# Performance work log

Measured on AMD Instinct MI355X. Metric: run time of the kernel, lower is better.

The kernel has to match this reference:

```python
import jax, jax.numpy as jnp
import numpy as np
from jax import lax

H, I, N, R, K, B, L = 2048, 4096, 16, 128, 4, 1, 2048

def silu(v):
    return v * jax.nn.sigmoid(v)

def setup_inputs() -> dict:
    key = jax.random.key(0)
    ks = jax.random.split(key, 8)
    f = jnp.float32
    x = jax.random.normal(ks[0], (B, L, H), f)
    W_in = jax.random.normal(ks[1], (H, 2 * I), f) / np.sqrt(H).astype(np.float32)
    conv_w = jax.random.normal(ks[2], (I, 1, K), f) / np.sqrt(K).astype(np.float32)  # OIH depthwise
    conv_b = jnp.zeros((I,), f)
    W_x = jax.random.normal(ks[3], (I, R + 2 * N), f) / np.sqrt(I).astype(np.float32)
    W_dt = jax.random.normal(ks[4], (R, I), f) / np.sqrt(R).astype(np.float32)
    # dt bias init as in Mamba: inverse-softplus of log-uniform dt
    dt = jnp.clip(jnp.exp(jax.random.normal(ks[5], (I,), f) * (np.log(0.1) - np.log(0.001)).astype(np.float32) + np.float32(np.log(0.001))), 1e-4, 0.1)
    b_dt = dt + jnp.log(-jnp.expm1(-dt))
    W_out = jax.random.normal(ks[6], (I, H), f) / np.sqrt(I).astype(np.float32)
    A_log = jnp.log(jnp.broadcast_to(jnp.arange(1, N + 1, dtype=f), (I, N)))
    D = jnp.ones((I,), f)
    return {"x": x, "W_in": W_in, "conv_w": conv_w, "conv_b": conv_b, "W_x": W_x,
            "W_dt": W_dt, "b_dt": b_dt, "W_out": W_out, "A_log": A_log, "D": D}

def reference(x, W_in, conv_w, conv_b, W_x, W_dt, b_dt, W_out, A_log, D):
    Bsz, Lq, _ = x.shape
    proj = jnp.swapaxes(x @ W_in, 1, 2)            # [B, 2I, L]
    h, gate = jnp.split(proj, 2, axis=1)           # each [B, I, L]
    # depthwise causal conv1d (pad K-1 both sides, truncate to L)
    h = lax.conv_general_dilated(h, conv_w, (1,), ((K - 1, K - 1),), feature_group_count=I)[..., :Lq]
    h = silu(h + conv_b[None, :, None])            # [B, I, L]
    ssm = jnp.swapaxes(h, 1, 2) @ W_x              # [B, L, R+2N]
    dt, Bm, Cm = jnp.split(ssm, [R, R + N], axis=-1)
    dt = jax.nn.softplus(dt @ W_dt + b_dt)         # [B, L, I]
    dt = jnp.swapaxes(dt, 1, 2)                    # [B, I, L]
    A = -jnp.exp(A_log)                            # [I, N]
    dA = jnp.exp(A[None, :, None, :] * dt[..., None])          # [B, I, L, N]
    dBu = dt[..., None] * Bm[:, None, :, :] * h[..., None]     # [B, I, L, N]

    def step(s, inp):
        dA_t, dBu_t, C_t = inp                     # [B,I,N],[B,I,N],[B,N]
        s = dA_t * s + dBu_t
        y = jnp.einsum('bin,bn->bi', s, C_t)
        return s, y

    s0 = jnp.zeros((Bsz, I, N), x.dtype)
    _, ys = lax.scan(step, s0, (jnp.moveaxis(dA, 2, 0), jnp.moveaxis(dBu, 2, 0), jnp.swapaxes(Cm, 0, 1)))
    y = jnp.moveaxis(ys, 0, 2)                     # [B, I, L]
    y = (y + h * D[None, :, None]) * silu(gate)
    return jnp.swapaxes(y, 1, 2) @ W_out           # [B, L, H]
```

## Files before the change

kernel.cpp:

```cpp
#include <hip/hip_runtime.h>

typedef unsigned short u16;
typedef unsigned int u32;
typedef __attribute__((ext_vector_type(2))) float f32x2;
typedef __attribute__((ext_vector_type(4))) float f32x4;
typedef __attribute__((ext_vector_type(8))) short s16x8;
typedef __attribute__((ext_vector_type(4))) u16 u16x4;

static constexpr int Hdim = 2048, Idim = 4096, Ndim = 16, Rdim = 128, Lseq = 2048;
static constexpr int NCH = 64, LCH = 32;

__device__ __forceinline__ u16 f2bf(float f) {
  u32 u = __builtin_bit_cast(u32, f);
  u += 0x7fffu + ((u >> 16) & 1u);
  return (u16)(u >> 16);
}
__device__ __forceinline__ float bf2f(u16 u) {
  u32 x = ((u32)u) << 16;
  return __builtin_bit_cast(float, x);
}

__global__ void k_cvt(const float* __restrict__ src, u16* __restrict__ dst, int n4) {
  int i = blockIdx.x * blockDim.x + threadIdx.x;
  if (i >= n4) return;
  f32x4 v = ((const f32x4*)src)[i];
  u16x4 o = {f2bf(v.x), f2bf(v.y), f2bf(v.z), f2bf(v.w)};
  ((u16x4*)dst)[i] = o;
}

__global__ void k_tcvt(const float* __restrict__ src, u16* __restrict__ dst,
                       int R, int C, int dstld) {
  __shared__ float tile[32][33];
  int tx = threadIdx.x & 31, ty = threadIdx.x >> 5;
  int c0 = blockIdx.x * 32, r0 = blockIdx.y * 32;
#pragma unroll
  for (int j = 0; j < 32; j += 8) {
    int r = r0 + ty + j, c = c0 + tx;
    tile[ty + j][tx] = (r < R && c < C) ? src[(size_t)r * C + c] : 0.f;
  }
  __syncthreads();
#pragma unroll
  for (int j = 0; j < 32; j += 8) {
    int c = c0 + ty + j, r = r0 + tx;
    if (c < C && r < R) dst[(size_t)c * dstld + r] = f2bf(tile[tx][ty + j]);
  }
}

__global__ __launch_bounds__(256)
void k_tcvt64(const float* __restrict__ src, u16* __restrict__ dst, int C, int ld) {
  __shared__ u16 tile[64][68];
  const int c0 = blockIdx.x * 64, r0 = blockIdx.y * 64;
#pragma unroll
  for (int it = 0; it < 4; ++it) {
    int v = it * 256 + threadIdx.x;
    int row = v >> 4, c4 = v & 15;
    f32x4 d = *(const f32x4*)&src[(size_t)(r0 + row) * C + c0 + c4 * 4];
    u16x4 o = {f2bf(d.x), f2bf(d.y), f2bf(d.z), f2bf(d.w)};
    *(u16x4*)&tile[row][c4 * 4] = o;
  }
  __syncthreads();
#pragma unroll
  for (int it = 0; it < 4; ++it) {
    int v = it * 256 + threadIdx.x;
    int oc = v >> 4, r4 = v & 15;
    u16x4 o = {tile[r4 * 4 + 0][oc], tile[r4 * 4 + 1][oc],
               tile[r4 * 4 + 2][oc], tile[r4 * 4 + 3][oc]};
    *(u16x4*)&dst[(size_t)(c0 + oc) * ld + r0 + r4 * 4] = o;
  }
}

__global__ void k_conv(const u16* __restrict__ projb, const float* __restrict__ cw,
                       const float* __restrict__ cb, u16* __restrict__ hcb) {
  int idx = blockIdx.x * 256 + threadIdx.x;
  int i = idx & (Idim - 1), l = idx >> 12;
  float acc = cb[i];
#pragma unroll
  for (int k = 0; k < 4; ++k) {
    int lk = l - 3 + k;
    if (lk >= 0) acc += cw[i * 4 + k] * bf2f(projb[(size_t)lk * (2 * Idim) + i]);
  }
  float s = acc * (1.f / (1.f + __expf(-acc)));
  hcb[idx] = f2bf(s);
}

__global__ __launch_bounds__(256)
void k_red3(const float* __restrict__ Cp, float* __restrict__ ssm, u16* __restrict__ dtr) {
  int i = blockIdx.x * 256 + threadIdx.x;
  f32x4 s = {0.f, 0.f, 0.f, 0.f};
#pragma unroll
  for (int z = 0; z < 8; ++z) {
    f32x4 v = ((const f32x4*)(Cp + (size_t)z * Lseq * 256))[i];
    s.x += v.x; s.y += v.y; s.z += v.z; s.w += v.w;
  }
  ((f32x4*)ssm)[i] = s;
  int l = i >> 6, c4 = i & 63;
  if (c4 < 32) {
    u16x4 o = {f2bf(s.x), f2bf(s.y), f2bf(s.z), f2bf(s.w)};
    *(u16x4*)&dtr[(size_t)l * 128 + c4 * 4] = o;
  }
}

__global__ __launch_bounds__(256)
void k_red5(const float* __restrict__ Cp, float* __restrict__ out) {
  int i = blockIdx.x * 256 + threadIdx.x;
  const size_t S = (size_t)Lseq * Hdim;
  f32x4 a = ((const f32x4*)Cp)[i];
  f32x4 b = ((const f32x4*)(Cp + S))[i];
  f32x4 c = ((const f32x4*)(Cp + 2 * S))[i];
  f32x4 d = ((const f32x4*)(Cp + 3 * S))[i];
  f32x4 r = {(a.x + b.x) + (c.x + d.x), (a.y + b.y) + (c.y + d.y),
             (a.z + b.z) + (c.z + d.z), (a.w + b.w) + (c.w + d.w)};
  ((f32x4*)out)[i] = r;
}

__global__ __launch_bounds__(256)
void k_scan1(const u16* __restrict__ dtfb, const u16* __restrict__ hcb,
             const float* __restrict__ ssm, const float* __restrict__ A_log,
             float* __restrict__ Sloc, float* __restrict__ dtsum) {
  __shared__ float Bs[LCH][16];
  const int c = blockIdx.y;
  const int i = blockIdx.x * 256 + threadIdx.x;
  const int l0 = c * LCH;
  {
    int t = threadIdx.x;
    int l = t >> 3, q = t & 7;
    *(f32x2*)&Bs[l][q * 2] = *(const f32x2*)&ssm[(size_t)(l0 + l) * 256 + 128 + q * 2];
  }
  float a[16];
#pragma unroll
  for (int n4 = 0; n4 < 4; ++n4) {
    f32x4 v = *(const f32x4*)&A_log[(size_t)i * 16 + n4 * 4];
    a[n4 * 4 + 0] = -__expf(v.x);
    a[n4 * 4 + 1] = -__expf(v.y);
    a[n4 * 4 + 2] = -__expf(v.z);
    a[n4 * 4 + 3] = -__expf(v.w);
  }
  __syncthreads();
  float s[16];
#pragma unroll
  for (int n = 0; n < 16; ++n) s[n] = 0.f;
  float dsum = 0.f;
  for (int l = 0; l < LCH; ++l) {
    float dtv = bf2f(dtfb[(size_t)(l0 + l) * Idim + i]);
    float hv = bf2f(hcb[(size_t)(l0 + l) * Idim + i]);
    dsum += dtv;
    float dh = dtv * hv;
#pragma unroll
    for (int n = 0; n < 16; ++n) {
      float dA = __expf(a[n] * dtv);
      s[n] = dA * s[n] + dh * Bs[l][n];
    }
  }
#pragma unroll
  for (int n4 = 0; n4 < 4; ++n4) {
    f32x4 v = {s[n4 * 4], s[n4 * 4 + 1], s[n4 * 4 + 2], s[n4 * 4 + 3]};
    *(f32x4*)&Sloc[((size_t)c * Idim + i) * 16 + n4 * 4] = v;
  }
  dtsum[(size_t)c * Idim + i] = dsum;
}

__global__ __launch_bounds__(256)
void k_scan2(const float* __restrict__ Sloc, const float* __restrict__ dtsum,
             const float* __restrict__ A_log, float* __restrict__ sinit) {
  const int idx = blockIdx.x * 256 + threadIdx.x;
  const float a = -__expf(A_log[idx]);
  const int i = idx >> 4;
  float acc = 0.f;
  for (int c = 0; c < NCH; ++c) {
    size_t o = (size_t)c * (Idim * 16) + idx;
    sinit[o] = acc;
    acc = __expf(a * dtsum[(size_t)c * Idim + i]) * acc + Sloc[o];
  }
}

__global__ __launch_bounds__(256)
void k_scan3(const u16* __restrict__ dtfb, const u16* __restrict__ hcb,
             const float* __restrict__ ssm, const float* __restrict__ A_log,
             const float* __restrict__ Dp, const u16* __restrict__ projb,
             const float* __restrict__ sinit, u16* __restrict__ yb) {
  __shared__ float SBC[LCH][32];
  const int c = blockIdx.y;
  const int i = blockIdx.x * 256 + threadIdx.x;
  const int l0 = c * LCH;
  {
    int t = threadIdx.x;
    int l = t >> 3, q = t & 7;
    *(f32x4*)&SBC[l][q * 4] = *(const f32x4*)&ssm[(size_t)(l0 + l) * 256 + 128 + q * 4];
  }
  float a[16], s[16];
#pragma unroll
  for (int n4 = 0; n4 < 4; ++n4) {
    f32x4 v = *(const f32x4*)&A_log[(size_t)i * 16 + n4 * 4];
    a[n4 * 4 + 0] = -__expf(v.x);
    a[n4 * 4 + 1] = -__expf(v.y);
    a[n4 * 4 + 2] = -__expf(v.z);
    a[n4 * 4 + 3] = -__expf(v.w);
    f32x4 sv = *(const f32x4*)&sinit[((size_t)c * Idim + i) * 16 + n4 * 4];
    s[n4 * 4 + 0] = sv.x;
    s[n4 * 4 + 1] = sv.y;
    s[n4 * 4 + 2] = sv.z;
    s[n4 * 4 + 3] = sv.w;
  }
  const float Di = Dp[i];
  __syncthreads();
  for (int l = 0; l < LCH; ++l) {
    float dtv = bf2f(dtfb[(size_t)(l0 + l) * Idim + i]);
    float hv = bf2f(hcb[(size_t)(l0 + l) * Idim + i]);
    float dh = dtv * hv;
    float y = 0.f;
#pragma unroll
    for (int n = 0; n < 16; ++n) {
      float dA = __expf(a[n] * dtv);
      s[n] = dA * s[n] + dh * SBC[l][n];
      y += s[n] * SBC[l][16 + n];
    }
    float g = bf2f(projb[(size_t)(l0 + l) * (2 * Idim) + Idim + i]);
    y = (y + hv * Di) * (g / (1.f + __expf(-g)));
    yb[(size_t)(l0 + l) * Idim + i] = f2bf(y);
  }
}

__device__ __forceinline__ void gload_lds16(const void* g, void* l) {
  __builtin_amdgcn_global_load_lds((const __attribute__((address_space(1))) void*)g,
                                   (__attribute__((address_space(3))) void*)l, 16, 0, 0);
}

template <int EPI>
__device__ __forceinline__ void gemm_body(const u16* __restrict__ A, const u16* __restrict__ Bt,
                                          float* __restrict__ C, u16* __restrict__ Caux,
                                          int N, int K, int kchunk,
                                          const float* __restrict__ bias,
                                          int m0, int n0, int kz) {
  __shared__ u16 As[128 * 32];
  __shared__ u16 Bs[128 * 32];
  const int tid = threadIdx.x;
  const int wave = tid >> 6, lane = tid & 63;
  const int wm = (wave >> 1) * 64, wn = (wave & 1) * 64;
  const int lr = lane >> 2;
  const int lc = lane & 3;
  const int arow = wave * 32;

  f32x4 acc[4][4];
#pragma unroll
  for (int a = 0; a < 4; ++a)
#pragma unroll
    for (int b = 0; b < 4; ++b) acc[a][b] = (f32x4){0.f, 0.f, 0.f, 0.f};

  const int k_begin = kz * kchunk;
  const int k_end = k_begin + kchunk;

  for (int k = k_begin; k < k_end; k += 32) {
#pragma unroll
    for (int j = 0; j < 2; ++j) {
      const u16* ga = A + (size_t)(m0 + arow + j * 16 + lr) * K + k + lc * 8;
      gload_lds16(ga, &As[(arow + j * 16) * 32]);
      const u16* gb = Bt + (size_t)(n0 + arow + j * 16 + lr) * K + k + lc * 8;
      gload_lds16(gb, &Bs[(arow + j * 16) * 32]);
    }
    __syncthreads();
    const int kh = (lane >> 4) * 8;
    const int fr = lane & 15;
    s16x8 af[4], bfr[4];
#pragma unroll
    for (int f = 0; f < 4; ++f) {
      af[f] = *(const s16x8*)&As[(wm + f * 16 + fr) * 32 + kh];
      bfr[f] = *(const s16x8*)&Bs[(wn + f * 16 + fr) * 32 + kh];
    }
#pragma unroll
    for (int fm = 0; fm < 4; ++fm)
#pragma unroll
      for (int fn = 0; fn < 4; ++fn)
        acc[fm][fn] = __builtin_amdgcn_mfma_f32_16x16x32_bf16(af[fm], bfr[fn], acc[fm][fn], 0, 0, 0);
    __syncthreads();
  }

  const int cr = (lane >> 4) * 4, cc = lane & 15;
#pragma unroll
  for (int fm = 0; fm < 4; ++fm)
#pragma unroll
    for (int fn = 0; fn < 4; ++fn)
#pragma unroll
      for (int j = 0; j < 4; ++j) {
        int row = m0 + wm + fm * 16 + cr + j;
        int col = n0 + wn + fn * 16 + cc;
        float v = acc[fm][fn][j];
        if (EPI == 0) {
          C[(size_t)row * N + col] = v;
        } else {
          float xv = v + bias[col];
          Caux[(size_t)row * N + col] = f2bf(fmaxf(xv, 0.f) + log1pf(__expf(-fabsf(xv))));
        }
      }
}

__global__ __launch_bounds__(256)
void k_gemm3(const u16* __restrict__ A, const u16* __restrict__ Bt, float* __restrict__ Cp) {
  gemm_body<0>(A, Bt, Cp + (size_t)blockIdx.z * Lseq * 256, nullptr, 256, Idim, Idim / 8,
               nullptr, blockIdx.x * 128, blockIdx.y * 128, blockIdx.z);
}

__global__ __launch_bounds__(256)
void k_gemm4(const u16* __restrict__ A, const u16* __restrict__ Bt, u16* __restrict__ Caux,
             const float* __restrict__ bias) {
  gemm_body<5>(A, Bt, nullptr, Caux, Idim, Rdim, Rdim, bias,
               blockIdx.x * 128, blockIdx.y * 128, 0);
}

__device__ __forceinline__ void g8_stage(const u16* __restrict__ g, int ld, int row0, int kcol,
                                         u16* lds, int slot, int wid, int lane) {
#pragma unroll
  for (int j = 0; j < 2; ++j) {
    const u16* ga = g + (size_t)(row0 + j * 64 + wid * 8 + (lane >> 3)) * ld
                      + kcol + (((lane & 7) ^ (lane >> 3)) << 3);
    gload_lds16(ga, &lds[slot + j * 4096 + wid * 512]);
  }
}

#define ASLOT(buf, h) (((buf)*2 + (h)) * 8192)
#define BSLOT(buf, h) (32768 + ((buf)*2 + (h)) * 8192)

template <int BUF, int MH, int NH>
__device__ __forceinline__ void g8_compute(const u16* lds, f32x4 (&acc)[2][4][2][2],
                                           int qm, int qn, int lane) {
  const int r16 = lane & 15, kq = lane >> 4;
  s16x8 af[4][2], bq[2][2];
#pragma unroll
  for (int fm = 0; fm < 4; ++fm) {
    int row = qm * 64 + fm * 16 + r16;
#pragma unroll
    for (int ks = 0; ks < 2; ++ks) {
      int ch = (ks * 4 + kq) ^ (row & 7);
      af[fm][ks] = *(const s16x8*)&lds[ASLOT(BUF, MH) + row * 64 + ch * 8];
    }
  }
#pragma unroll
  for (int fn = 0; fn < 2; ++fn) {
    int row = qn * 32 + fn * 16 + r16;
#pragma unroll
    for (int ks = 0; ks < 2; ++ks) {
      int ch = (ks * 4 + kq) ^ (row & 7);
      bq[fn][ks] = *(const s16x8*)&lds[BSLOT(BUF, NH) + row * 64 + ch * 8];
    }
  }
  __builtin_amdgcn_s_setprio(1);
#pragma unroll
  for (int fm = 0; fm < 4; ++fm)
#pragma unroll
    for (int fn = 0; fn < 2; ++fn)
#pragma unroll
      for (int ks = 0; ks < 2; ++ks)
        acc[MH][fm][NH][fn] =
            __builtin_amdgcn_mfma_f32_16x16x32_bf16(af[fm][ks], bq[fn][ks], acc[MH][fm][NH][fn], 0, 0, 0);
  __builtin_amdgcn_s_setprio(0);
}

#define G8BAR()                         \
  do {                                  \
    __builtin_amdgcn_s_barrier();       \
    __builtin_amdgcn_sched_barrier(0);  \
  } while (0)
#define G8VM4() asm volatile("s_waitcnt vmcnt(4)" ::: "memory")

template <int KLD, int NITER, int OUTLD, int EPI>
__device__ __forceinline__ void g8p_body(const u16* __restrict__ A, const u16* __restrict__ Bt,
                                         float* __restrict__ Cf, u16* __restrict__ Cb,
                                         int m0, int n0, int kbase) {
  extern __shared__ u16 lds[];
  const int tid = threadIdx.x, wid = tid >> 6, lane = tid & 63;
  const int qm = wid >> 2, qn = wid & 3;

  f32x4 acc[2][4][2][2];
#pragma unroll
  for (int a = 0; a < 2; ++a)
#pragma unroll
    for (int b = 0; b < 4; ++b)
#pragma unroll
      for (int c = 0; c < 2; ++c)
#pragma unroll
        for (int d = 0; d < 2; ++d) acc[a][b][c][d] = (f32x4){0.f, 0.f, 0.f, 0.f};

  g8_stage(A, KLD, m0, kbase, lds, ASLOT(0, 0), wid, lane);
  g8_stage(Bt, KLD, n0 + 128, kbase, lds, BSLOT(0, 1), wid, lane);
  g8_stage(A, KLD, m0 + 128, kbase, lds, ASLOT(0, 1), wid, lane);
  g8_stage(Bt, KLD, n0, kbase, lds, BSLOT(0, 0), wid, lane);
  g8_stage(A, KLD, m0, kbase + 64, lds, ASLOT(1, 0), wid, lane);
  g8_stage(Bt, KLD, n0 + 128, kbase + 64, lds, BSLOT(1, 1), wid, lane);

  for (int i = 0; i < NITER - 1; ++i) {
    const int kc0 = kbase + i * 128, kc2 = kc0 + 128, kc3 = kc0 + 192;
    g8_stage(A, KLD, m0 + 128, kc0 + 64, lds, ASLOT(1, 1), wid, lane);
    G8VM4();
    G8BAR();
    g8_compute<0, 0, 0>(lds, acc, qm, qn, lane);
    G8BAR();
    g8_stage(Bt, KLD, n0, kc0 + 64, lds, BSLOT(1, 0), wid, lane);
    G8BAR();
    g8_compute<0, 0, 1>(lds, acc, qm, qn, lane);
    G8BAR();
    g8_stage(A, KLD, m0, kc2, lds, ASLOT(0, 0), wid, lane);
    G8BAR();
    g8_compute<0, 1, 1>(lds, acc, qm, qn, lane);
    G8BAR();
    g8_stage(Bt, KLD, n0 + 128, kc2, lds, BSLOT(0, 1), wid, lane);
    G8BAR();
    g8_compute<0, 1, 0>(lds, acc, qm, qn, lane);
    G8BAR();
    g8_stage(A, KLD, m0 + 128, kc2, lds, ASLOT(0, 1), wid, lane);
    G8VM4();
    G8BAR();
    g8_compute<1, 0, 0>(lds, acc, qm, qn, lane);
    G8BAR();
    g8_stage(Bt, KLD, n0, kc2, lds, BSLOT(0, 0), wid, lane);
    G8BAR();
    g8_compute<1, 0, 1>(lds, acc, qm, qn, lane);
    G8BAR();
    g8_stage(A, KLD, m0, kc3, lds, ASLOT(1, 0), wid, lane);
    G8BAR();
    g8_compute<1, 1, 1>(lds, acc, qm, qn, lane);
    G8BAR();
    g8_stage(Bt, KLD, n0 + 128, kc3, lds, BSLOT(1, 1), wid, lane);
    G8BAR();
    g8_compute<1, 1, 0>(lds, acc, qm, qn, lane);
    G8BAR();
  }

  g8_stage(A, KLD, m0 + 128, kbase + (2 * NITER - 1) * 64, lds, ASLOT(1, 1), wid, lane);
  g8_stage(Bt, KLD, n0, kbase + (2 * NITER - 1) * 64, lds, BSLOT(1, 0), wid, lane);
  asm volatile("s_waitcnt vmcnt(0)" ::: "memory");
  G8BAR();
  g8_compute<0, 0, 0>(lds, acc, qm, qn, lane);
  g8_compute<0, 0, 1>(lds, acc, qm, qn, lane);
  g8_compute<0, 1, 1>(lds, acc, qm, qn, lane);
  g8_compute<0, 1, 0>(lds, acc, qm, qn, lane);
  g8_compute<1, 0, 0>(lds, acc, qm, qn, lane);
  g8_compute<1, 0, 1>(lds, acc, qm, qn, lane);
  g8_compute<1, 1, 1>(lds, acc, qm, qn, lane);
  g8_compute<1, 1, 0>(lds, acc, qm, qn, lane);

  const int cr = (lane >> 4) * 4, cc = lane & 15;
#pragma unroll
  for (int mh = 0; mh < 2; ++mh)
#pragma unroll
    for (int fm = 0; fm < 4; ++fm)
#pragma unroll
      for (int nh = 0; nh < 2; ++nh)
#pragma unroll
        for (int fn = 0; fn < 2; ++fn)
#pragma unroll
          for (int j = 0; j < 4; ++j) {
            int row = m0 + mh * 128 + qm * 64 + fm * 16 + cr + j;
            int col = n0 + nh * 128 + qn * 32 + fn * 16 + cc;
            float v = acc[mh][fm][nh][fn][j];
            if (EPI == 0) Cb[(size_t)row * OUTLD + col] = f2bf(v);
            else Cf[(size_t)row * OUTLD + col] = v;
          }
}

__global__ __launch_bounds__(512, 2)
void k_gemm1_8p(const u16* __restrict__ A, const u16* __restrict__ Bt, u16* __restrict__ Cb) {
  const int m0 = (int)(blockIdx.x >> 5) * 256, n0 = (int)(blockIdx.x & 31) * 256;
  g8p_body<2048, 16, 8192, 0>(A, Bt, nullptr, Cb, m0, n0, 0);
}

__global__ __launch_bounds__(512, 2)
void k_gemm5_8p(const u16* __restrict__ A, const u16* __restrict__ Bt, float* __restrict__ Cp) {
  int bid = blockIdx.x;
  int wg = (bid & 7) * 8 + (bid >> 3);
  int m0 = (wg >> 3) * 256, n0 = (wg & 7) * 256;
  float* Cf = Cp + (size_t)blockIdx.y * Lseq * Hdim;
  g8p_body<4096, 8, 2048, 1>(A, Bt, Cf, nullptr, m0, n0, (int)blockIdx.y * 1024);
}

extern "C" void kernel_launch(void* const* d_in, const int* in_sizes, int n_in,
                              void* d_out, int out_size, void* d_ws, size_t ws_size,
                              hipStream_t stream) {
  const float* x = (const float*)d_in[0];
  const float* W_in = (const float*)d_in[1];
  const float* convw = (const float*)d_in[2];
  const float* convb = (const float*)d_in[3];
  const float* W_x = (const float*)d_in[4];
  const float* W_dt = (const float*)d_in[5];
  const float* b_dt = (const float*)d_in[6];
  const float* W_out = (const float*)d_in[7];
  const float* A_log = (const float*)d_in[8];
  const float* Dp = (const float*)d_in[9];
  float* out = (float*)d_out;

  char* w = (char*)d_ws;
  const size_t OFF_PROJ = 0;
  const size_t OFF_HC = OFF_PROJ + (size_t)Lseq * 2 * Idim * 4;
  const size_t OFF_DT = OFF_HC + (size_t)Lseq * Idim * 4;
  const size_t OFF_XB = OFF_DT + (size_t)Lseq * Idim * 4;
  const size_t OFF_WIN = OFF_XB + (size_t)Lseq * Hdim * 2;
  const size_t OFF_WOUT = OFF_WIN + (size_t)2 * Idim * Hdim * 2;
  const size_t OFF_HCB = OFF_WOUT + (size_t)Hdim * Idim * 2;
  const size_t OFF_YB = OFF_HCB + (size_t)Lseq * Idim * 2;
  const size_t OFF_WX = OFF_YB + (size_t)Lseq * Idim * 2;
  const size_t OFF_WDT = OFF_WX + (size_t)256 * Idim * 2;
  const size_t OFF_SSM = OFF_WDT + (size_t)Idim * Rdim * 2;
  const size_t OFF_DTR = OFF_SSM + (size_t)Lseq * 256 * 4;

  u16* projb = (u16*)(w + OFF_PROJ);
  u16* dtfb = (u16*)(w + OFF_DT);
  u16* xb = (u16*)(w + OFF_XB);
  u16* winT = (u16*)(w + OFF_WIN);
  u16* woutT = (u16*)(w + OFF_WOUT);
  u16* hcb = (u16*)(w + OFF_HCB);
  u16* yb = (u16*)(w + OFF_YB);
  u16* wxt = (u16*)(w + OFF_WX);
  u16* wdtT = (u16*)(w + OFF_WDT);
  float* ssm = (float*)(w + OFF_SSM);
  u16* dtr = (u16*)(w + OFF_DTR);
  float* Cpart3 = (float*)(w + OFF_HC);
  float* Sloc = (float*)(w + OFF_HC);
  float* sinit = (float*)(w + OFF_WIN);
  float* dtsum = (float*)(w + OFF_WIN + (size_t)16 * 1024 * 1024);
  float* Cpart5 = (float*)(w + OFF_PROJ);

  hipMemsetAsync(wxt, 0, (size_t)256 * Idim * 2, stream);

  k_cvt<<<(Lseq * Hdim / 4 + 255) / 256, 256, 0, stream>>>(x, xb, Lseq * Hdim / 4);
  k_tcvt64<<<dim3(2 * Idim / 64, Hdim / 64), 256, 0, stream>>>(W_in, winT, 2 * Idim, Hdim);
  k_tcvt<<<dim3(5, Idim / 32), 256, 0, stream>>>(W_x, wxt, Idim, 160, Idim);
  k_tcvt64<<<dim3(Idim / 64, Rdim / 64), 256, 0, stream>>>(W_dt, wdtT, Idim, Rdim);
  k_tcvt64<<<dim3(Hdim / 64, Idim / 64), 256, 0, stream>>>(W_out, woutT, Hdim, Idim);

  hipFuncSetAttribute((const void*)k_gemm1_8p, hipFuncAttributeMaxDynamicSharedMemorySize, 131072);
  k_gemm1_8p<<<256, 512, 131072, stream>>>(xb, winT, projb);

  k_conv<<<(size_t)Lseq * Idim / 256, 256, 0, stream>>>(projb, convw, convb, hcb);

  k_gemm3<<<dim3(Lseq / 128, 2, 8), 256, 0, stream>>>(hcb, wxt, Cpart3);
  k_red3<<<Lseq * 64 / 256, 256, 0, stream>>>(Cpart3, ssm, dtr);

  k_gemm4<<<dim3(Lseq / 128, Idim / 128), 256, 0, stream>>>(dtr, wdtT, dtfb, b_dt);

  k_scan1<<<dim3(Idim / 256, NCH), 256, 0, stream>>>(dtfb, hcb, ssm, A_log, Sloc, dtsum);
  k_scan2<<<Idim * 16 / 256, 256, 0, stream>>>(Sloc, dtsum, A_log, sinit);
  k_scan3<<<dim3(Idim / 256, NCH), 256, 0, stream>>>(dtfb, hcb, ssm, A_log, Dp, projb, sinit, yb);

  hipFuncSetAttribute((const void*)k_gemm5_8p, hipFuncAttributeMaxDynamicSharedMemorySize, 131072);
  k_gemm5_8p<<<dim3(64, 4), 512, 131072, stream>>>(yb, woutT, Cpart5);
  k_red5<<<Lseq * Hdim / 4 / 256, 256, 0, stream>>>(Cpart5, out);
}
```

Baseline: 459.4 us.

## Fuse prep conversions into one kernel and fold split-K reductions into GEMMs

Merges the five input/weight conversion kernels into a single block-dispatched prep kernel. It also removes the separate split-K reduction kernels for gemm3 and gemm5: the last-arriving block per output tile, found with an atomic counter, sums the partials and writes ssm/dtr or the final output. This cuts kernel launches and an extra pass over the partials, but adds threadfences, atomics and a serial tail inside the GEMMs. The counters are cleared by an enlarged memset.

```diff
diff --git a/kernel.cpp b/kernel.cpp
--- a/kernel.cpp
+++ b/kernel.cpp
@@ -20,36 +20,10 @@
   return __builtin_bit_cast(float, x);
 }
 
-__global__ void k_cvt(const float* __restrict__ src, u16* __restrict__ dst, int n4) {
-  int i = blockIdx.x * blockDim.x + threadIdx.x;
-  if (i >= n4) return;
-  f32x4 v = ((const f32x4*)src)[i];
-  u16x4 o = {f2bf(v.x), f2bf(v.y), f2bf(v.z), f2bf(v.w)};
-  ((u16x4*)dst)[i] = o;
-}
-
-__global__ void k_tcvt(const float* __restrict__ src, u16* __restrict__ dst,
-                       int R, int C, int dstld) {
-  __shared__ float tile[32][33];
-  int tx = threadIdx.x & 31, ty = threadIdx.x >> 5;
-  int c0 = blockIdx.x * 32, r0 = blockIdx.y * 32;
-#pragma unroll
-  for (int j = 0; j < 32; j += 8) {
-    int r = r0 + ty + j, c = c0 + tx;
-    tile[ty + j][tx] = (r < R && c < C) ? src[(size_t)r * C + c] : 0.f;
-  }
-  __syncthreads();
-#pragma unroll
-  for (int j = 0; j < 32; j += 8) {
-    int c = c0 + ty + j, r = r0 + tx;
-    if (c < C && r < R) dst[(size_t)c * dstld + r] = f2bf(tile[tx][ty + j]);
-  }
-}
-
-__global__ __launch_bounds__(256)
-void k_tcvt64(const float* __restrict__ src, u16* __restrict__ dst, int C, int ld) {
-  __shared__ u16 tile[64][68];
-  const int c0 = blockIdx.x * 64, r0 = blockIdx.y * 64;
+__device__ __forceinline__ void tcvt64_body(const float* __restrict__ src, u16* __restrict__ dst,
+                                            int C, int ld, int bx, int by, void* smem) {
+  u16(*tile)[68] = (u16(*)[68])smem;
+  const int c0 = bx * 64, r0 = by * 64;
 #pragma unroll
   for (int it = 0; it < 4; ++it) {
     int v = it * 256 + threadIdx.x;
@@ -69,6 +43,57 @@
   }
 }
 
+__device__ __forceinline__ void tcvt_body(const float* __restrict__ src, u16* __restrict__ dst,
+                                          int R, int C, int dstld, int bx, int by, void* smem) {
+  float(*tile)[33] = (float(*)[33])smem;
+  int tx = threadIdx.x & 31, ty = threadIdx.x >> 5;
+  int c0 = bx * 32, r0 = by * 32;
+#pragma unroll
+  for (int j = 0; j < 32; j += 8) {
+    int r = r0 + ty + j, c = c0 + tx;
+    tile[ty + j][tx] = (r < R && c < C) ? src[(size_t)r * C + c] : 0.f;
+  }
+  __syncthreads();
+#pragma unroll
+  for (int j = 0; j < 32; j += 8) {
+    int c = c0 + ty + j, r = r0 + tx;
+    if (c < C && r < R) dst[(size_t)c * dstld + r] = f2bf(tile[tx][ty + j]);
+  }
+}
+
+static constexpr int PREP_BLOCKS = 2048 + 4096 + 640 + 128 + 2048;
+
+__global__ __launch_bounds__(256)
+void k_prep(const float* __restrict__ x, u16* __restrict__ xb,
+            const float* __restrict__ W_in, u16* __restrict__ winT,
+            const float* __restrict__ W_x, u16* __restrict__ wxt,
+            const float* __restrict__ W_dt, u16* __restrict__ wdtT,
+            const float* __restrict__ W_out, u16* __restrict__ woutT) {
+  __shared__ char smem[64 * 68 * 2];
+  int bid = blockIdx.x;
+  if (bid < 2048) {
+    int i = bid * 512 + threadIdx.x;
+#pragma unroll
+    for (int t = 0; t < 2; ++t) {
+      f32x4 v = ((const f32x4*)x)[i + t * 256];
+      u16x4 o = {f2bf(v.x), f2bf(v.y), f2bf(v.z), f2bf(v.w)};
+      ((u16x4*)xb)[i + t * 256] = o;
+    }
+  } else if (bid < 6144) {
+    int sub = bid - 2048;
+    tcvt64_body(W_in, winT, 2 * Idim, Hdim, sub & 127, sub >> 7, smem);
+  } else if (bid < 6784) {
+    int sub = bid - 6144;
+    tcvt_body(W_x, wxt, Idim, 160, Idim, sub % 5, sub / 5, smem);
+  } else if (bid < 6912) {
+    int sub = bid - 6784;
+    tcvt64_body(W_dt, wdtT, Idim, Rdim, sub & 63, sub >> 6, smem);
+  } else {
+    int sub = bid - 6912;
+    tcvt64_body(W_out, woutT, Hdim, Idim, sub & 31, sub >> 5, smem);
+  }
+}
+
 __global__ void k_conv(const u16* __restrict__ projb, const float* __restrict__ cw,
                        const float* __restrict__ cb, u16* __restrict__ hcb) {
   int idx = blockIdx.x * 256 + threadIdx.x;
@@ -81,36 +106,6 @@
   }
   float s = acc * (1.f / (1.f + __expf(-acc)));
   hcb[idx] = f2bf(s);
-}
-
-__global__ __launch_bounds__(256)
-void k_red3(const float* __restrict__ Cp, float* __restrict__ ssm, u16* __restrict__ dtr) {
-  int i = blockIdx.x * 256 + threadIdx.x;
-  f32x4 s = {0.f, 0.f, 0.f, 0.f};
-#pragma unroll
-  for (int z = 0; z < 8; ++z) {
-    f32x4 v = ((const f32x4*)(Cp + (size_t)z * Lseq * 256))[i];
-    s.x += v.x; s.y += v.y; s.z += v.z; s.w += v.w;
-  }
-  ((f32x4*)ssm)[i] = s;
-  int l = i >> 6, c4 = i & 63;
-  if (c4 < 32) {
-    u16x4 o = {f2bf(s.x), f2bf(s.y), f2bf(s.z), f2bf(s.w)};
-    *(u16x4*)&dtr[(size_t)l * 128 + c4 * 4] = o;
-  }
-}
-
-__global__ __launch_bounds__(256)
-void k_red5(const float* __restrict__ Cp, float* __restrict__ out) {
-  int i = blockIdx.x * 256 + threadIdx.x;
-  const size_t S = (size_t)Lseq * Hdim;
-  f32x4 a = ((const f32x4*)Cp)[i];
-  f32x4 b = ((const f32x4*)(Cp + S))[i];
-  f32x4 c = ((const f32x4*)(Cp + 2 * S))[i];
-  f32x4 d = ((const f32x4*)(Cp + 3 * S))[i];
-  f32x4 r = {(a.x + b.x) + (c.x + d.x), (a.y + b.y) + (c.y + d.y),
-             (a.z + b.z) + (c.z + d.z), (a.w + b.w) + (c.w + d.w)};
-  ((f32x4*)out)[i] = r;
 }
 
 __global__ __launch_bounds__(256)
@@ -294,9 +289,39 @@
 }
 
 __global__ __launch_bounds__(256)
-void k_gemm3(const u16* __restrict__ A, const u16* __restrict__ Bt, float* __restrict__ Cp) {
+void k_gemm3(const u16* __restrict__ A, const u16* __restrict__ Bt, float* __restrict__ Cp,
+             float* __restrict__ ssm, u16* __restrict__ dtr, u32* __restrict__ cnt) {
   gemm_body<0>(A, Bt, Cp + (size_t)blockIdx.z * Lseq * 256, nullptr, 256, Idim, Idim / 8,
                nullptr, blockIdx.x * 128, blockIdx.y * 128, blockIdx.z);
+  __threadfence();
+  __syncthreads();
+  __shared__ u32 last;
+  if (threadIdx.x == 0) {
+    u32 old = atomicAdd(&cnt[blockIdx.y * 16 + blockIdx.x], 1u);
+    last = (old == 7u);
+  }
+  __syncthreads();
+  if (!last) return;
+  __threadfence();
+  const int r0 = blockIdx.x * 128, c0 = blockIdx.y * 128;
+#pragma unroll
+  for (int j = 0; j < 16; ++j) {
+    int pos = j * 256 + threadIdx.x;
+    int r = pos >> 5, cv = pos & 31;
+    size_t off = (size_t)(r0 + r) * 256 + c0 + cv * 4;
+    f32x4 s = {0.f, 0.f, 0.f, 0.f};
+#pragma unroll
+    for (int z = 0; z < 8; ++z) {
+      f32x4 v = *(const f32x4*)&Cp[(size_t)z * Lseq * 256 + off];
+      s.x += v.x; s.y += v.y; s.z += v.z; s.w += v.w;
+    }
+    if (blockIdx.y == 0) {
+      u16x4 o = {f2bf(s.x), f2bf(s.y), f2bf(s.z), f2bf(s.w)};
+      *(u16x4*)&dtr[(size_t)(r0 + r) * 128 + cv * 4] = o;
+    } else {
+      *(f32x4*)&ssm[off] = s;
+    }
+  }
 }
 
 __global__ __launch_bounds__(256)
@@ -463,12 +488,38 @@
 }
 
 __global__ __launch_bounds__(512, 2)
-void k_gemm5_8p(const u16* __restrict__ A, const u16* __restrict__ Bt, float* __restrict__ Cp) {
+void k_gemm5_8p(const u16* __restrict__ A, const u16* __restrict__ Bt, float* __restrict__ Cp,
+                float* __restrict__ out, u32* __restrict__ cnt) {
   int bid = blockIdx.x;
   int wg = (bid & 7) * 8 + (bid >> 3);
   int m0 = (wg >> 3) * 256, n0 = (wg & 7) * 256;
   float* Cf = Cp + (size_t)blockIdx.y * Lseq * Hdim;
   g8p_body<4096, 8, 2048, 1>(A, Bt, Cf, nullptr, m0, n0, (int)blockIdx.y * 1024);
+
+  __threadfence();
+  __syncthreads();
+  __shared__ u32 last;
+  if (threadIdx.x == 0) {
+    u32 old = atomicAdd(&cnt[bid], 1u);
+    last = (old == 3u);
+  }
+  __syncthreads();
+  if (!last) return;
+  __threadfence();
+  const size_t S = (size_t)Lseq * Hdim;
+#pragma unroll
+  for (int j = 0; j < 32; ++j) {
+    int pos = j * 512 + threadIdx.x;
+    int r = pos >> 6, cv = pos & 63;
+    size_t off = (size_t)(m0 + r) * Hdim + n0 + cv * 4;
+    f32x4 a = *(const f32x4*)&Cp[off];
+    f32x4 b = *(const f32x4*)&Cp[S + off];
+    f32x4 c = *(const f32x4*)&Cp[2 * S + off];
+    f32x4 d = *(const f32x4*)&Cp[3 * S + off];
+    f32x4 r4 = {(a.x + b.x) + (c.x + d.x), (a.y + b.y) + (c.y + d.y),
+                (a.z + b.z) + (c.z + d.z), (a.w + b.w) + (c.w + d.w)};
+    *(f32x4*)&out[off] = r4;
+  }
 }
 
 extern "C" void kernel_launch(void* const* d_in, const int* in_sizes, int n_in,
@@ -499,6 +550,7 @@
   const size_t OFF_WDT = OFF_WX + (size_t)256 * Idim * 2;
   const size_t OFF_SSM = OFF_WDT + (size_t)Idim * Rdim * 2;
   const size_t OFF_DTR = OFF_SSM + (size_t)Lseq * 256 * 4;
+  const size_t OFF_CNT = OFF_DTR + (size_t)Lseq * 128 * 2;
 
   u16* projb = (u16*)(w + OFF_PROJ);
   u16* dtfb = (u16*)(w + OFF_DT);
@@ -511,27 +563,24 @@
   u16* wdtT = (u16*)(w + OFF_WDT);
   float* ssm = (float*)(w + OFF_SSM);
   u16* dtr = (u16*)(w + OFF_DTR);
+  u32* cnt3 = (u32*)(w + OFF_CNT);
+  u32* cnt5 = (u32*)(w + OFF_CNT + 256);
   float* Cpart3 = (float*)(w + OFF_HC);
   float* Sloc = (float*)(w + OFF_HC);
   float* sinit = (float*)(w + OFF_WIN);
   float* dtsum = (float*)(w + OFF_WIN + (size_t)16 * 1024 * 1024);
   float* Cpart5 = (float*)(w + OFF_PROJ);
 
-  hipMemsetAsync(wxt, 0, (size_t)256 * Idim * 2, stream);
-
-  k_cvt<<<(Lseq * Hdim / 4 + 255) / 256, 256, 0, stream>>>(x, xb, Lseq * Hdim / 4);
-  k_tcvt64<<<dim3(2 * Idim / 64, Hdim / 64), 256, 0, stream>>>(W_in, winT, 2 * Idim, Hdim);
-  k_tcvt<<<dim3(5, Idim / 32), 256, 0, stream>>>(W_x, wxt, Idim, 160, Idim);
-  k_tcvt64<<<dim3(Idim / 64, Rdim / 64), 256, 0, stream>>>(W_dt, wdtT, Idim, Rdim);
-  k_tcvt64<<<dim3(Hdim / 64, Idim / 64), 256, 0, stream>>>(W_out, woutT, Hdim, Idim);
+  hipMemsetAsync(w + OFF_WX, 0, (OFF_CNT + 1024) - OFF_WX, stream);
+
+  k_prep<<<PREP_BLOCKS, 256, 0, stream>>>(x, xb, W_in, winT, W_x, wxt, W_dt, wdtT, W_out, woutT);
 
   hipFuncSetAttribute((const void*)k_gemm1_8p, hipFuncAttributeMaxDynamicSharedMemorySize, 131072);
   k_gemm1_8p<<<256, 512, 131072, stream>>>(xb, winT, projb);
 
   k_conv<<<(size_t)Lseq * Idim / 256, 256, 0, stream>>>(projb, convw, convb, hcb);
 
-  k_gemm3<<<dim3(Lseq / 128, 2, 8), 256, 0, stream>>>(hcb, wxt, Cpart3);
-  k_red3<<<Lseq * 64 / 256, 256, 0, stream>>>(Cpart3, ssm, dtr);
+  k_gemm3<<<dim3(Lseq / 128, 2, 8), 256, 0, stream>>>(hcb, wxt, Cpart3, ssm, dtr, cnt3);
 
   k_gemm4<<<dim3(Lseq / 128, Idim / 128), 256, 0, stream>>>(dtr, wdtT, dtfb, b_dt);
 
@@ -540,6 +589,5 @@
   k_scan3<<<dim3(Idim / 256, NCH), 256, 0, stream>>>(dtfb, hcb, ssm, A_log, Dp, projb, sinit, yb);
 
   hipFuncSetAttribute((const void*)k_gemm5_8p, hipFuncAttributeMaxDynamicSharedMemorySize, 131072);
-  k_gemm5_8p<<<dim3(64, 4), 512, 131072, stream>>>(yb, woutT, Cpart5);
-  k_red5<<<Lseq * Hdim / 4 / 256, 256, 0, stream>>>(Cpart5, out);
-}
+  k_gemm5_8p<<<dim3(64, 4), 512, 131072, stream>>>(yb, woutT, Cpart5, out, cnt5);
+}
```

New measurement: 754.5 us. +64.2%, slower.
